# Performance work log

Hardware: AMD Instinct MI355X
Metric: run time of the kernel (lower is better)

## Reference

```python
import jax, jax.numpy as jnp
import numpy as np

NEG_SLOPE = 0.2  # PyG GATv2Conv default negative_slope


def gatv2_layer(x, Wl, Wr, att, bias, src, dst, N, H, C):
    # x: [N, F_in]; Wl, Wr: [F_in, H*C]; att: [H, C]; bias: [H*C]
    xl = (x @ Wl).reshape(N, H, C)  # source transform (lin_l)
    xr = (x @ Wr).reshape(N, H, C)  # target transform (lin_r)
    # per-edge GATv2 score: a^T LeakyReLU(xl[j] + xr[i])
    e = jax.nn.leaky_relu(xl[src] + xr[dst], NEG_SLOPE)      # [E, H, C]
    logits = jnp.einsum('ehc,hc->eh', e, att)                # [E, H]
    # segment softmax over incoming edges of each destination node
    m = jax.ops.segment_max(logits, dst, num_segments=N)     # [N, H]
    p = jnp.exp(logits - m[dst])                             # [E, H]
    s = jax.ops.segment_sum(p, dst, num_segments=N)          # [N, H]
    alpha = p / s[dst]                                       # [E, H]
    out = jax.ops.segment_sum(xl[src] * alpha[..., None], dst, num_segments=N)  # [N, H, C]
    return out.reshape(N, H * C) + bias


def setup_inputs() -> dict:
    key = jax.random.key(0)
    ks = jax.random.split(key, 12)
    B, N, F_IN = 1, 100000, 128
    E, H, C = 1600000, 4, 16
    D = H * C  # 64
    x = jax.random.normal(ks[0], (B, N, F_IN), dtype=jnp.float32)
    edge_index = jax.random.randint(ks[1], (2, E), 0, N, dtype=jnp.int32)
    def glorot(k, shape):
        fan_in, fan_out = shape[0], shape[1]
        lim = (6.0 / (fan_in + fan_out)) ** 0.5
        return jax.random.uniform(k, shape, jnp.float32, -lim, lim)
    # layer 1: F_IN -> H*C ; layer 2: H*C -> H*C
    W1l = glorot(ks[2], (F_IN, D))
    W1r = glorot(ks[3], (F_IN, D))
    att1 = glorot(ks[4], (H, C))
    b1 = jnp.zeros((D,), jnp.float32)
    W2l = glorot(ks[5], (D, D))
    W2r = glorot(ks[6], (D, D))
    att2 = glorot(ks[7], (H, C))
    b2 = jnp.zeros((D,), jnp.float32)
    return {"x": x, "edge_index": edge_index,
            "W1l": W1l, "W1r": W1r, "att1": att1, "b1": b1,
            "W2l": W2l, "W2r": W2r, "att2": att2, "b2": b2}


def reference(x, edge_index, W1l, W1r, att1, b1, W2l, W2r, att2, b2):
    B, N_per, F = x.shape
    N = B * N_per
    H, C = att1.shape
    h = x.reshape(N, F)
    # PyG GATv2Conv adds self-loops by default
    loops = jnp.arange(N, dtype=edge_index.dtype)
    src = jnp.concatenate([edge_index[0], loops])
    dst = jnp.concatenate([edge_index[1], loops])
    h = jax.nn.relu(gatv2_layer(h, W1l, W1r, att1, b1, src, dst, N, H, C))
    # dropout is identity in eval mode
    h = jax.nn.relu(gatv2_layer(h, W2l, W2r, att2, b2, src, dst, N, H, C))
    return h.reshape(B, N_per, -1)
```

## Files before the change

### kernel.cpp

```cpp
#include <hip/hip_runtime.h>
#include <hip/hip_bf16.h>


typedef unsigned long long u64;

#define NBLK_S 512
#define LOG2E 1.44269504f

template <int CTRL>
__device__ __forceinline__ float add_ror(float v) {
    int r = __builtin_amdgcn_update_dpp(0, __float_as_int(v), CTRL, 0xF, 0xF, true);
    return v + __int_as_float(r);
}
__device__ __forceinline__ float head_sum16(float v) {
    v = add_ror<0x121>(v);
    v = add_ror<0x122>(v);
    v = add_ror<0x124>(v);
    v = add_ror<0x128>(v);
    return v;
}

__global__ __launch_bounds__(256) void hist_fused(const int* __restrict__ edst,
                                                  int* __restrict__ deg,
                                                  int* __restrict__ gh, int E, int nW) {
    __shared__ int h[256];
    for (int i = threadIdx.x; i < 256; i += 256) h[i] = 0;
    __syncthreads();
    const int chunk = (E + NBLK_S - 1) / NBLK_S;
    const int lo = blockIdx.x * chunk;
    const int hi = min(E, lo + chunk);
    for (int i = lo + threadIdx.x; i < hi; i += 256) {
        int d = edst[i];
        atomicAdd(&deg[d], 1);
        atomicAdd(&h[d >> 9], 1);
    }
    __syncthreads();
    for (int w = threadIdx.x; w < nW; w += 256)
        gh[w * NBLK_S + blockIdx.x] = h[w];
}

__global__ void scan_a(const int* __restrict__ deg, int* __restrict__ incl,
                       int* __restrict__ partials, int n) {
    __shared__ int sm[2][1024];
    int tid = threadIdx.x;
    int i = blockIdx.x * 1024 + tid;
    int v = (i < n) ? deg[i] : 0;
    sm[0][tid] = v;
    __syncthreads();
    int pin = 0;
    #pragma unroll
    for (int ofs = 1; ofs < 1024; ofs <<= 1) {
        int pout = pin ^ 1;
        sm[pout][tid] = sm[pin][tid] + ((tid >= ofs) ? sm[pin][tid - ofs] : 0);
        pin = pout;
        __syncthreads();
    }
    int r = sm[pin][tid];
    if (i < n) incl[i] = r;
    if (tid == 1023) partials[blockIdx.x] = r;
}

__global__ void scan_b(int* partials, int nblk) {
    __shared__ int sm[2][1024];
    int tid = threadIdx.x;
    int v = (tid < nblk) ? partials[tid] : 0;
    sm[0][tid] = v;
    __syncthreads();
    int pin = 0;
    #pragma unroll
    for (int ofs = 1; ofs < 1024; ofs <<= 1) {
        int pout = pin ^ 1;
        sm[pout][tid] = sm[pin][tid] + ((tid >= ofs) ? sm[pin][tid - ofs] : 0);
        pin = pout;
        __syncthreads();
    }
    if (tid < nblk) partials[tid] = sm[pin][tid] - v;
}

__global__ void scan_c(const int* __restrict__ deg, const int* __restrict__ incl,
                       const int* __restrict__ partials, int* __restrict__ offs,
                       int n, int E) {
    int i = blockIdx.x * blockDim.x + threadIdx.x;
    if (i < n) offs[i] = partials[i >> 10] + incl[i] - deg[i];
    if (i == 0) offs[n] = E;
}

__global__ __launch_bounds__(NBLK_S) void sort_scan(const int* __restrict__ offs,
                                                    int* __restrict__ gh, int N) {
    __shared__ int sm[2][NBLK_S];
    const int w = blockIdx.x;
    const int t = threadIdx.x;
    int v = gh[w * NBLK_S + t];
    sm[0][t] = v;
    __syncthreads();
    int pin = 0;
    #pragma unroll
    for (int ofs = 1; ofs < NBLK_S; ofs <<= 1) {
        int pout = pin ^ 1;
        sm[pout][t] = sm[pin][t] + ((t >= ofs) ? sm[pin][t - ofs] : 0);
        pin = pout;
        __syncthreads();
    }
    gh[w * NBLK_S + t] = offs[w << 9] + sm[pin][t] - v;
}

#define WIDX(c) ((c) + (((c) >> 5) << 2))
#define GEMM_LDS_FLOATS (64 * 140 + 64 * 68)

template <int K>
__device__ __forceinline__ void gemm_body(int rbase, const float* __restrict__ X,
                                          const float* __restrict__ Wl,
                                          const float* __restrict__ Wr,
                                          float* __restrict__ xl,
                                          float* __restrict__ xr, int N,
                                          float* __restrict__ sm) {
    constexpr int KT = 64;
    constexpr int LDW = 140;
    constexpr int LDX = KT + 4;
    float* Ws = sm;
    float* Xs = sm + KT * LDW;
    const int tid = threadIdx.x;
    const int tx = tid & 15;
    const int ty = tid >> 4;
    const int c0 = tx * 8;
    const int wc = WIDX(c0);

    float acc[4][8];
    #pragma unroll
    for (int j = 0; j < 4; ++j)
        #pragma unroll
        for (int i = 0; i < 8; ++i) acc[j][i] = 0.f;

    #pragma unroll
    for (int t = 0; t < K / KT; ++t) {
        if (t) __syncthreads();
        for (int f = tid; f < KT * 16; f += 256) {
            int k = f >> 4;
            int c = (f & 15) << 2;
            float4 a = *reinterpret_cast<const float4*>(&Wl[(size_t)(t * KT + k) * 64 + c]);
            float4 b = *reinterpret_cast<const float4*>(&Wr[(size_t)(t * KT + k) * 64 + c]);
            *reinterpret_cast<float4*>(&Ws[k * LDW + WIDX(c)]) = a;
            *reinterpret_cast<float4*>(&Ws[k * LDW + WIDX(64 + c)]) = b;
        }
        for (int f = tid; f < 64 * (KT / 4); f += 256) {
            int m = f >> 4;
            int k4 = (f & 15) << 2;
            int r = rbase + m;
            float4 v = (r < N) ? *reinterpret_cast<const float4*>(&X[(size_t)r * K + t * KT + k4])
                               : make_float4(0.f, 0.f, 0.f, 0.f);
            *reinterpret_cast<float4*>(&Xs[m * LDX + k4]) = v;
        }
        __syncthreads();

        #pragma unroll 2
        for (int k4 = 0; k4 < KT; k4 += 4) {
            float4 xv[4];
            #pragma unroll
            for (int j = 0; j < 4; ++j)
                xv[j] = *reinterpret_cast<const float4*>(&Xs[(ty + 16 * j) * LDX + k4]);
            #pragma unroll
            for (int kk = 0; kk < 4; ++kk) {
                float4 w0 = *reinterpret_cast<const float4*>(&Ws[(k4 + kk) * LDW + wc]);
                float4 w1 = *reinterpret_cast<const float4*>(&Ws[(k4 + kk) * LDW + wc + 4]);
                float w[8] = {w0.x, w0.y, w0.z, w0.w, w1.x, w1.y, w1.z, w1.w};
                #pragma unroll
                for (int j = 0; j < 4; ++j) {
                    float xk = (kk == 0) ? xv[j].x : (kk == 1) ? xv[j].y
                             : (kk == 2) ? xv[j].z : xv[j].w;
                    #pragma unroll
                    for (int i = 0; i < 8; ++i)
                        acc[j][i] = fmaf(xk, w[i], acc[j][i]);
                }
            }
        }
    }

    float* op = (c0 < 64) ? xl : xr;
    const int cc = c0 & 63;
    #pragma unroll
    for (int j = 0; j < 4; ++j) {
        int r = rbase + ty + 16 * j;
        if (r < N) {
            float4 v0 = make_float4(acc[j][0], acc[j][1], acc[j][2], acc[j][3]);
            float4 v1 = make_float4(acc[j][4], acc[j][5], acc[j][6], acc[j][7]);
            *reinterpret_cast<float4*>(&op[(size_t)r * 64 + cc]) = v0;
            *reinterpret_cast<float4*>(&op[(size_t)r * 64 + cc + 4]) = v1;
        }
    }
}

__global__ __launch_bounds__(256) void place_gemm(const int* __restrict__ esrc,
                                                  const int* __restrict__ edst,
                                                  const int* __restrict__ gh,
                                                  unsigned* __restrict__ pairs,
                                                  int E, int nW,
                                                  const float* __restrict__ X,
                                                  const float* __restrict__ Wl,
                                                  const float* __restrict__ Wr,
                                                  float* __restrict__ xl,
                                                  float* __restrict__ xr, int N) {
    __shared__ float sm[GEMM_LDS_FLOATS];
    if (blockIdx.x < NBLK_S) {
        int* cur = (int*)sm;
        const int bid = blockIdx.x;
        for (int i = threadIdx.x; i < nW; i += 256)
            cur[i] = gh[i * NBLK_S + bid];
        __syncthreads();
        const int chunk = (E + NBLK_S - 1) / NBLK_S;
        const int lo = bid * chunk;
        const int hi = min(E, lo + chunk);
        for (int i = lo + threadIdx.x; i < hi; i += 256) {
            int d = edst[i];
            int s = esrc[i];
            int pos = atomicAdd(&cur[d >> 9], 1);
            pairs[pos] = ((unsigned)(d & 511) << 17) | (unsigned)s;
        }
    } else {
        gemm_body<128>((blockIdx.x - NBLK_S) * 64, X, Wl, Wr, xl, xr, N, sm);
    }
}

__global__ __launch_bounds__(256) void scatter_gemm(const unsigned* __restrict__ pairs,
                                                    const int* __restrict__ offs,
                                                    int* __restrict__ srcs, int nW, int gemmBase,
                                                    const float* __restrict__ X,
                                                    const float* __restrict__ Wl,
                                                    const float* __restrict__ Wr,
                                                    float* __restrict__ xl,
                                                    float* __restrict__ xr, int N) {
    __shared__ float sm[GEMM_LDS_FLOATS];
    if ((int)blockIdx.x < nW) {
        int* cur = (int*)sm;
        int w = blockIdx.x;
        int d0 = w << 9;
        int nd = min(512, N - d0);
        for (int i = threadIdx.x; i < nd; i += 256) cur[i] = offs[d0 + i];
        __syncthreads();
        int p0 = offs[d0];
        int p1 = offs[min(d0 + 512, N)];
        for (int idx = p0 + threadIdx.x; idx < p1; idx += 256) {
            unsigned pr = pairs[idx];
            int doff = (int)(pr >> 17);
            int s = (int)(pr & 0x1FFFFu);
            int pos = atomicAdd(&cur[doff], 1);
            srcs[pos] = s << 6;
        }
    } else {
        gemm_body<128>((gemmBase + blockIdx.x - nW) * 64, X, Wl, Wr, xl, xr, N, sm);
    }
}

template <int K>
__global__ __launch_bounds__(256) void gemm_lr(const float* __restrict__ X,
                                               const float* __restrict__ Wl,
                                               const float* __restrict__ Wr,
                                               float* __restrict__ xl,
                                               float* __restrict__ xr, int N) {
    __shared__ float sm[GEMM_LDS_FLOATS];
    gemm_body<K>(blockIdx.x * 64, X, Wl, Wr, xl, xr, N, sm);
}

__global__ __launch_bounds__(256) void gat_kernel(const float* __restrict__ xl,
                                                  const float* __restrict__ xr,
                                                  const int* __restrict__ offs,
                                                  const int* __restrict__ srcs,
                                                  const float* __restrict__ att,
                                                  const float* __restrict__ bias,
                                                  float* __restrict__ out, int N) {
    int lane = threadIdx.x & 63;
    int wid = threadIdx.x >> 6;
    int n = blockIdx.x * 4 + wid;
    if (n >= N) return;
    float a_l = att[lane] * LOG2E;
    float a1 = 0.6f * a_l;
    float a2 = 0.4f * a_l;
    float b_l = bias[lane];
    unsigned bn = (unsigned)n * 64u + (unsigned)lane;
    float xr_d = xr[bn];
    float xls = xl[bn];
    float u = xls + xr_d;
    float p = exp2f(head_sum16(fmaf(a1, u, a2 * fabsf(u))));
    float s0 = p, s1 = 0.f, s2 = 0.f, s3 = 0.f;
    float o0 = xls * p, o1 = 0.f, o2 = 0.f, o3 = 0.f;
    int e0 = offs[n], e1 = offs[n + 1];
    int j = e0;
    int ja = min((e0 + 3) & ~3, e1);
    for (; j < ja; ++j) {
        unsigned off = (unsigned)srcs[j] + lane;
        float xa = xl[off];
        float ua = xa + xr_d;
        float pa = exp2f(head_sum16(fmaf(a1, ua, a2 * fabsf(ua))));
        s1 += pa;
        o1 = fmaf(xa, pa, o1);
    }
    for (; j + 3 < e1; j += 4) {
        int4 q = *reinterpret_cast<const int4*>(&srcs[j]);
        float xa = xl[(unsigned)q.x + lane];
        float xb = xl[(unsigned)q.y + lane];
        float xc = xl[(unsigned)q.z + lane];
        float xd = xl[(unsigned)q.w + lane];
        float ua = xa + xr_d, ub = xb + xr_d, uc = xc + xr_d, ud = xd + xr_d;
        float pa = exp2f(head_sum16(fmaf(a1, ua, a2 * fabsf(ua))));
        float pb = exp2f(head_sum16(fmaf(a1, ub, a2 * fabsf(ub))));
        float pc = exp2f(head_sum16(fmaf(a1, uc, a2 * fabsf(uc))));
        float pd = exp2f(head_sum16(fmaf(a1, ud, a2 * fabsf(ud))));
        s0 += pa; s1 += pb; s2 += pc; s3 += pd;
        o0 = fmaf(xa, pa, o0);
        o1 = fmaf(xb, pb, o1);
        o2 = fmaf(xc, pc, o2);
        o3 = fmaf(xd, pd, o3);
    }
    for (; j < e1; ++j) {
        unsigned off = (unsigned)srcs[j] + lane;
        float xa = xl[off];
        float ua = xa + xr_d;
        float pa = exp2f(head_sum16(fmaf(a1, ua, a2 * fabsf(ua))));
        s1 += pa;
        o1 = fmaf(xa, pa, o1);
    }
    float s = (s0 + s1) + (s2 + s3);
    float o = (o0 + o1) + (o2 + o3);
    out[bn] = fmaxf(o / s + b_l, 0.f);
}

extern "C" void kernel_launch(void* const* d_in, const int* in_sizes, int n_in,
                              void* d_out, int out_size, void* d_ws, size_t ws_size,
                              hipStream_t stream) {
    const float* x    = (const float*)d_in[0];
    const int*   edge = (const int*)d_in[1];
    const float* W1l  = (const float*)d_in[2];
    const float* W1r  = (const float*)d_in[3];
    const float* att1 = (const float*)d_in[4];
    const float* b1   = (const float*)d_in[5];
    const float* W2l  = (const float*)d_in[6];
    const float* W2r  = (const float*)d_in[7];
    const float* att2 = (const float*)d_in[8];
    const float* b2   = (const float*)d_in[9];

    const int N = in_sizes[0] / 128;
    const int E = in_sizes[1] / 2;
    const int* esrc = edge;
    const int* edst = edge + E;

    char* ws = (char*)d_ws;
    size_t off = 0;
    auto alloc = [&](size_t bytes) {
        void* p = ws + off;
        off += (bytes + 255) & ~(size_t)255;
        return p;
    };
    float* xl     = (float*)alloc((size_t)N * 64 * 4);
    float* xr     = (float*)alloc((size_t)N * 64 * 4);
    float* h      = (float*)alloc((size_t)N * 64 * 4);
    int* deg      = (int*)alloc((size_t)N * 4);
    int* incl     = (int*)alloc((size_t)N * 4);
    int* offs     = (int*)alloc((size_t)(N + 1) * 4);
    int* partials = (int*)alloc(1024 * 4);
    int* srcs     = (int*)alloc((size_t)E * 4);
    unsigned* pairs = (unsigned*)alloc((size_t)E * 4);
    int* gh       = (int*)alloc((size_t)256 * NBLK_S * 4);
    (void)ws_size;

    hipMemsetAsync(deg, 0, (size_t)N * 4, stream);

    const int nblk = (N + 1023) >> 10;
    const int nW = (N + 511) >> 9;
    const int gblk = (N + 63) / 64;
    const int GA = gblk / 2;
    const int GB = gblk - GA;

    hist_fused<<<NBLK_S, 256, 0, stream>>>(edst, deg, gh, E, nW);
    scan_a<<<nblk, 1024, 0, stream>>>(deg, incl, partials, N);
    scan_b<<<1, 1024, 0, stream>>>(partials, nblk);
    scan_c<<<(N + 255) / 256, 256, 0, stream>>>(deg, incl, partials, offs, N, E);
    sort_scan<<<nW, NBLK_S, 0, stream>>>(offs, gh, N);
    place_gemm<<<NBLK_S + GA, 256, 0, stream>>>(esrc, edst, gh, pairs, E, nW,
                                                x, W1l, W1r, xl, xr, N);
    scatter_gemm<<<nW + GB, 256, 0, stream>>>(pairs, offs, srcs, nW, GA,
                                              x, W1l, W1r, xl, xr, N);
    gat_kernel<<<(N + 3) / 4, 256, 0, stream>>>(xl, xr, offs, srcs, att1, b1, h, N);
    gemm_lr<64><<<gblk, 256, 0, stream>>>(h, W2l, W2r, xl, xr, N);
    gat_kernel<<<(N + 3) / 4, 256, 0, stream>>>(xl, xr, offs, srcs, att2, b2, (float*)d_out, N);
}
```

Measured before the change: 460.6 us.

## Process four edges per wavefront with float4 gathers in GAT aggregation

The aggregation kernel now splits each 64-lane wavefront into four 16-lane groups, each handling a different edge and loading a full 64-float feature row as float4 per lane. The per-head reduction shrinks from a 16-lane DPP chain to a 4-lane quad sum. Per-group partial sums are combined with cross-group shuffles at the end. The goal is wider memory transactions and fewer dependent reduction steps per edge, at the cost of extra end-of-loop shuffles, a masked tail, and only a quarter of lanes writing the output.

```diff
diff --git a/kernel.cpp b/kernel.cpp
--- a/kernel.cpp
+++ b/kernel.cpp
@@ -7,16 +7,11 @@
 #define NBLK_S 512
 #define LOG2E 1.44269504f
 
-template <int CTRL>
-__device__ __forceinline__ float add_ror(float v) {
-    int r = __builtin_amdgcn_update_dpp(0, __float_as_int(v), CTRL, 0xF, 0xF, true);
-    return v + __int_as_float(r);
-}
-__device__ __forceinline__ float head_sum16(float v) {
-    v = add_ror<0x121>(v);
-    v = add_ror<0x122>(v);
-    v = add_ror<0x124>(v);
-    v = add_ror<0x128>(v);
+__device__ __forceinline__ float quad_sum4(float v) {
+    int r1 = __builtin_amdgcn_update_dpp(0, __float_as_int(v), 0xB1, 0xF, 0xF, true);
+    v += __int_as_float(r1);
+    int r2 = __builtin_amdgcn_update_dpp(0, __float_as_int(v), 0x4E, 0xF, 0xF, true);
+    v += __int_as_float(r2);
     return v;
 }
 
@@ -267,60 +262,80 @@
                                                   const float* __restrict__ att,
                                                   const float* __restrict__ bias,
                                                   float* __restrict__ out, int N) {
-    int lane = threadIdx.x & 63;
-    int wid = threadIdx.x >> 6;
-    int n = blockIdx.x * 4 + wid;
+    const int lane = threadIdx.x & 63;
+    const int wid = threadIdx.x >> 6;
+    const int n = blockIdx.x * 4 + wid;
     if (n >= N) return;
-    float a_l = att[lane] * LOG2E;
-    float a1 = 0.6f * a_l;
-    float a2 = 0.4f * a_l;
-    float b_l = bias[lane];
-    unsigned bn = (unsigned)n * 64u + (unsigned)lane;
-    float xr_d = xr[bn];
-    float xls = xl[bn];
-    float u = xls + xr_d;
-    float p = exp2f(head_sum16(fmaf(a1, u, a2 * fabsf(u))));
-    float s0 = p, s1 = 0.f, s2 = 0.f, s3 = 0.f;
-    float o0 = xls * p, o1 = 0.f, o2 = 0.f, o3 = 0.f;
-    int e0 = offs[n], e1 = offs[n + 1];
+    const int g = lane >> 4;
+    const int t = lane & 15;
+
+    const float4 av = *reinterpret_cast<const float4*>(att + 4 * t);
+    const float c1 = 0.6f * LOG2E, c2 = 0.4f * LOG2E;
+    const float a1x = c1 * av.x, a1y = c1 * av.y, a1z = c1 * av.z, a1w = c1 * av.w;
+    const float a2x = c2 * av.x, a2y = c2 * av.y, a2z = c2 * av.z, a2w = c2 * av.w;
+
+    const float4 xr4 = *reinterpret_cast<const float4*>(xr + (size_t)n * 64 + 4 * t);
+    const float4 xl4 = *reinterpret_cast<const float4*>(xl + (size_t)n * 64 + 4 * t);
+
+    float sacc = 0.f;
+    float ox = 0.f, oy = 0.f, oz = 0.f, ow = 0.f;
+
+    {
+        float ux = xl4.x + xr4.x, uy = xl4.y + xr4.y;
+        float uz = xl4.z + xr4.z, uw = xl4.w + xr4.w;
+        float l = fmaf(a1x, ux, a2x * fabsf(ux)) + fmaf(a1y, uy, a2y * fabsf(uy))
+                + fmaf(a1z, uz, a2z * fabsf(uz)) + fmaf(a1w, uw, a2w * fabsf(uw));
+        float p = exp2f(quad_sum4(l));
+        if (g == 0) {
+            sacc = p;
+            ox = xl4.x * p; oy = xl4.y * p; oz = xl4.z * p; ow = xl4.w * p;
+        }
+    }
+
+    const int e0 = offs[n], e1 = offs[n + 1];
     int j = e0;
-    int ja = min((e0 + 3) & ~3, e1);
-    for (; j < ja; ++j) {
-        unsigned off = (unsigned)srcs[j] + lane;
-        float xa = xl[off];
-        float ua = xa + xr_d;
-        float pa = exp2f(head_sum16(fmaf(a1, ua, a2 * fabsf(ua))));
-        s1 += pa;
-        o1 = fmaf(xa, pa, o1);
-    }
-    for (; j + 3 < e1; j += 4) {
-        int4 q = *reinterpret_cast<const int4*>(&srcs[j]);
-        float xa = xl[(unsigned)q.x + lane];
-        float xb = xl[(unsigned)q.y + lane];
-        float xc = xl[(unsigned)q.z + lane];
-        float xd = xl[(unsigned)q.w + lane];
-        float ua = xa + xr_d, ub = xb + xr_d, uc = xc + xr_d, ud = xd + xr_d;
-        float pa = exp2f(head_sum16(fmaf(a1, ua, a2 * fabsf(ua))));
-        float pb = exp2f(head_sum16(fmaf(a1, ub, a2 * fabsf(ub))));
-        float pc = exp2f(head_sum16(fmaf(a1, uc, a2 * fabsf(uc))));
-        float pd = exp2f(head_sum16(fmaf(a1, ud, a2 * fabsf(ud))));
-        s0 += pa; s1 += pb; s2 += pc; s3 += pd;
-        o0 = fmaf(xa, pa, o0);
-        o1 = fmaf(xb, pb, o1);
-        o2 = fmaf(xc, pc, o2);
-        o3 = fmaf(xd, pd, o3);
-    }
-    for (; j < e1; ++j) {
-        unsigned off = (unsigned)srcs[j] + lane;
-        float xa = xl[off];
-        float ua = xa + xr_d;
-        float pa = exp2f(head_sum16(fmaf(a1, ua, a2 * fabsf(ua))));
-        s1 += pa;
-        o1 = fmaf(xa, pa, o1);
-    }
-    float s = (s0 + s1) + (s2 + s3);
-    float o = (o0 + o1) + (o2 + o3);
-    out[bn] = fmaxf(o / s + b_l, 0.f);
+    for (; j + 4 <= e1; j += 4) {
+        int off = srcs[j + g];
+        const float4 xv = *reinterpret_cast<const float4*>(xl + off + 4 * t);
+        float ux = xv.x + xr4.x, uy = xv.y + xr4.y;
+        float uz = xv.z + xr4.z, uw = xv.w + xr4.w;
+        float l = fmaf(a1x, ux, a2x * fabsf(ux)) + fmaf(a1y, uy, a2y * fabsf(uy))
+                + fmaf(a1z, uz, a2z * fabsf(uz)) + fmaf(a1w, uw, a2w * fabsf(uw));
+        float p = exp2f(quad_sum4(l));
+        sacc += p;
+        ox = fmaf(xv.x, p, ox); oy = fmaf(xv.y, p, oy);
+        oz = fmaf(xv.z, p, oz); ow = fmaf(xv.w, p, ow);
+    }
+    const int rem = e1 - j;
+    if (rem > 0) {
+        int off = srcs[j + min(g, rem - 1)];
+        const float4 xv = *reinterpret_cast<const float4*>(xl + off + 4 * t);
+        float ux = xv.x + xr4.x, uy = xv.y + xr4.y;
+        float uz = xv.z + xr4.z, uw = xv.w + xr4.w;
+        float l = fmaf(a1x, ux, a2x * fabsf(ux)) + fmaf(a1y, uy, a2y * fabsf(uy))
+                + fmaf(a1z, uz, a2z * fabsf(uz)) + fmaf(a1w, uw, a2w * fabsf(uw));
+        float p = exp2f(quad_sum4(l));
+        if (g >= rem) p = 0.f;
+        sacc += p;
+        ox = fmaf(xv.x, p, ox); oy = fmaf(xv.y, p, oy);
+        oz = fmaf(xv.z, p, oz); ow = fmaf(xv.w, p, ow);
+    }
+
+    sacc += __shfl_xor(sacc, 16, 64); sacc += __shfl_xor(sacc, 32, 64);
+    ox += __shfl_xor(ox, 16, 64); ox += __shfl_xor(ox, 32, 64);
+    oy += __shfl_xor(oy, 16, 64); oy += __shfl_xor(oy, 32, 64);
+    oz += __shfl_xor(oz, 16, 64); oz += __shfl_xor(oz, 32, 64);
+    ow += __shfl_xor(ow, 16, 64); ow += __shfl_xor(ow, 32, 64);
+
+    if (g == 0) {
+        const float4 b4 = *reinterpret_cast<const float4*>(bias + 4 * t);
+        float inv = 1.f / sacc;
+        float4 r = make_float4(fmaxf(fmaf(ox, inv, b4.x), 0.f),
+                               fmaxf(fmaf(oy, inv, b4.y), 0.f),
+                               fmaxf(fmaf(oz, inv, b4.z), 0.f),
+                               fmaxf(fmaf(ow, inv, b4.w), 0.f));
+        *reinterpret_cast<float4*>(out + (size_t)n * 64 + 4 * t) = r;
+    }
 }
 
 extern "C" void kernel_launch(void* const* d_in, const int* in_sizes, int n_in,
```

Result: faster. 436.0 us (-5.3%).
